# Performance work log

Measured on AMD Instinct MI355X. Metric: run time of the kernel, lower is better.

Reference implementation:

```python
import jax, jax.numpy as jnp
import numpy as np


def _ternarize(p, delta, w):
    # {-w, 0, +w} via threshold mask, matching TrainableTernarize.forward
    return jnp.where(p > delta, w, jnp.where(p < -delta, -w, jnp.zeros_like(p)))


def _ternary_para(p, w):
    # TrainableTernaryPara.forward: delta = 0.05 * max|p|
    delta = 0.05 * jnp.max(jnp.abs(p))
    return _ternarize(p, delta, w)


def _init_scale(p):
    # w init: mean(|p|[|p| > 0.7 * mean|p|])
    a = jnp.abs(p)
    mask = (a > 0.7 * jnp.mean(a)).astype(p.dtype)
    return jnp.sum(a * mask) / jnp.sum(mask)


def setup_inputs() -> dict:
    key = jax.random.key(0)
    k1, k2, k3 = jax.random.split(key, 3)
    B, S, D_IN, D_OUT = 4, 2048, 4096, 4096
    x = jax.random.normal(k1, (B, S, D_IN), dtype=jnp.float32)
    bound = 1.0 / np.sqrt(D_IN)  # nn.Linear default init range
    W = jax.random.uniform(k2, (D_OUT, D_IN), minval=-bound, maxval=bound, dtype=jnp.float32)
    b = jax.random.uniform(k3, (D_OUT,), minval=-bound, maxval=bound, dtype=jnp.float32)
    w_scale = _init_scale(W)
    b_scale = _init_scale(b)
    return {"x": x, "W": W, "w_scale": w_scale, "b": b, "b_scale": b_scale}


def reference(x, W, w_scale, b, b_scale):
    Wt = _ternary_para(W, w_scale)   # [D_OUT, D_IN] in {-w,0,+w}
    bt = _ternary_para(b, b_scale)   # [D_OUT]
    # F.linear(x, Wt, bt) = x @ Wt.T + bt
    return jnp.einsum('bsi,oi->bso', x, Wt) + bt
```

## Files before the change

kernel.cpp:

```cpp
#include <hip/hip_runtime.h>

typedef int v4i __attribute__((ext_vector_type(4)));

#define BM 256
#define BN 256
#define BKB 64
#define NRING 4

#define GLOAD_LDS(gptr, lptr)                                                         \
  __builtin_amdgcn_global_load_lds(                                                   \
      (const __attribute__((address_space(1))) unsigned int*)(gptr),                  \
      (__attribute__((address_space(3))) unsigned int*)(lptr), 16, 0, 0)


__device__ __forceinline__ float max4abs(float4 v) {
  return fmaxf(fmaxf(fabsf(v.x), fabsf(v.y)), fmaxf(fabsf(v.z), fabsf(v.w)));
}

__device__ __forceinline__ int packq4(float4 v, float inv) {
  int b0 = ((int)fminf(127.f, fmaxf(-127.f, rintf(v.x * inv)))) & 255;
  int b1 = ((int)fminf(127.f, fmaxf(-127.f, rintf(v.y * inv)))) & 255;
  int b2 = ((int)fminf(127.f, fmaxf(-127.f, rintf(v.z * inv)))) & 255;
  int b3 = ((int)fminf(127.f, fmaxf(-127.f, rintf(v.w * inv)))) & 255;
  return b0 | (b1 << 8) | (b2 << 16) | (b3 << 24);
}

__global__ void prep1_kernel(const float4* __restrict__ X4,
                             signed char* __restrict__ Q,
                             float* __restrict__ sx, int K, int nrows,
                             const float4* __restrict__ W4, long nW4,
                             const float4* __restrict__ b4, int nb4,
                             unsigned* __restrict__ mx) {
  __shared__ float sm[4];
  const int tid = threadIdx.x;
  const int bid = blockIdx.x;

  if (bid < nrows) {
    const float4* xr = X4 + (size_t)bid * (K / 4);
    float4 v0 = xr[tid], v1 = xr[tid + 256], v2 = xr[tid + 512], v3 = xr[tid + 768];
    float m = fmaxf(fmaxf(max4abs(v0), max4abs(v1)), fmaxf(max4abs(v2), max4abs(v3)));
    for (int off = 32; off > 0; off >>= 1) m = fmaxf(m, __shfl_down(m, off));
    if ((tid & 63) == 0) sm[tid >> 6] = m;
    __syncthreads();
    const float total = fmaxf(fmaxf(sm[0], sm[1]), fmaxf(sm[2], sm[3]));
    const float inv = 127.f / total;
    int* qw = (int*)(Q + (size_t)bid * K);
    qw[tid]       = packq4(v0, inv);
    qw[tid + 256] = packq4(v1, inv);
    qw[tid + 512] = packq4(v2, inv);
    qw[tid + 768] = packq4(v3, inv);
    if (tid == 0) sx[bid] = total * (1.f / 127.f);
    return;
  }

  float m = 0.f;
  const bool isB = (bid == gridDim.x - 1);
  if (!isB) {
    const long wb = bid - nrows;
    const long stride = 1024L * blockDim.x;
    for (long i = wb * blockDim.x + tid; i < nW4; i += stride)
      m = fmaxf(m, max4abs(W4[i]));
  } else {
    for (int i = tid; i < nb4; i += blockDim.x) m = fmaxf(m, max4abs(b4[i]));
  }
  for (int off = 32; off > 0; off >>= 1) m = fmaxf(m, __shfl_down(m, off));
  if ((tid & 63) == 0) sm[tid >> 6] = m;
  __syncthreads();
  if (tid == 0) {
    m = fmaxf(fmaxf(sm[0], sm[1]), fmaxf(sm[2], sm[3]));
    atomicMax(mx + (isB ? 1 : 0), __float_as_uint(m));
  }
}

__global__ void prep_w_kernel(const float4* __restrict__ W4, long nW4,
                              const float4* __restrict__ b4, int nb4,
                              const unsigned* __restrict__ mx,
                              const float* __restrict__ bscale,
                              int* __restrict__ Twi, float4* __restrict__ bt) {
  if (blockIdx.x == gridDim.x - 1) {
    const float delta = 0.05f * __uint_as_float(mx[1]);
    const float s = *bscale;
    for (int i = threadIdx.x; i < nb4; i += blockDim.x) {
      float4 v = b4[i];
      float4 o;
      o.x = v.x > delta ? s : (v.x < -delta ? -s : 0.f);
      o.y = v.y > delta ? s : (v.y < -delta ? -s : 0.f);
      o.z = v.z > delta ? s : (v.z < -delta ? -s : 0.f);
      o.w = v.w > delta ? s : (v.w < -delta ? -s : 0.f);
      bt[i] = o;
    }
    return;
  }
  const float delta = 0.05f * __uint_as_float(mx[0]);
  const long stride = (long)(gridDim.x - 1) * blockDim.x;
  for (long i = blockIdx.x * (long)blockDim.x + threadIdx.x; i < nW4; i += stride) {
    float4 w = W4[i];
    int b0 = w.x > delta ? 1 : (w.x < -delta ? 0xFF : 0);
    int b1 = w.y > delta ? 1 : (w.y < -delta ? 0xFF : 0);
    int b2 = w.z > delta ? 1 : (w.z < -delta ? 0xFF : 0);
    int b3 = w.w > delta ? 1 : (w.w < -delta ? 0xFF : 0);
    Twi[i] = b0 | (b1 << 8) | (b2 << 16) | (b3 << 24);
  }
}

__global__ __launch_bounds__(512, 2) void gemm_tern_i8(
    const signed char* __restrict__ A,
    const signed char* __restrict__ B,
    const float* __restrict__ sx,
    const float* __restrict__ bt,
    const float* __restrict__ wsc,
    float* __restrict__ C,
    int M, int N, int K) {
  __shared__ __align__(16) signed char lds[NRING][2][BM * BKB];

  const int tid = threadIdx.x;
  const int wave = tid >> 6;
  const int lane = tid & 63;
  const int wm = wave >> 2, wn = wave & 3;
  const int quad = lane >> 4;
  const int l16 = lane & 15;

  const unsigned orig = blockIdx.x;
  const unsigned xcd = orig & 7;
  const unsigned r8 = orig >> 3;
  const int by = (int)(xcd * 4 + (r8 & 3));
  const int bx = (int)(r8 >> 2);
  const int bm0 = by * BM;
  const int bn0 = bx * BN;

  const signed char* gA[2];
  const signed char* gB[2];
#pragma unroll
  for (int j = 0; j < 2; ++j) {
    const int idx = j * 512 + tid;
    const int row = idx >> 2;
    const int gch = (idx & 3) ^ ((idx >> 3) & 3);
    gA[j] = A + (size_t)(bm0 + row) * K + gch * 16;
    gB[j] = B + (size_t)(bn0 + row) * K + gch * 16;
  }
  const int ldsbase = wave * 64 * 16;

#define STAGE_A(slot)                                \
  do {                                               \
    signed char* la = &lds[slot][0][ldsbase];        \
    GLOAD_LDS(gA[0], la);                            \
    GLOAD_LDS(gA[1], la + 8192);                     \
    gA[0] += BKB; gA[1] += BKB;                      \
  } while (0)
#define STAGE_B(slot)                                \
  do {                                               \
    signed char* lb = &lds[slot][1][ldsbase];        \
    GLOAD_LDS(gB[0], lb);                            \
    GLOAD_LDS(gB[1], lb + 8192);                     \
    gB[0] += BKB; gB[1] += BKB;                      \
  } while (0)

#define BAR()  do { __builtin_amdgcn_sched_barrier(0); __builtin_amdgcn_s_barrier(); \
                    __builtin_amdgcn_sched_barrier(0); } while (0)
#define WAITLGKM() do { asm volatile("s_waitcnt lgkmcnt(0)" ::: "memory");           \
                        __builtin_amdgcn_sched_barrier(0); } while (0)

  const int kchunk = quad ^ ((l16 >> 1) & 3);
  const int aoff = (wm * 128 + l16) * BKB + kchunk * 16;
  const int boff = (wn * 64 + l16) * BKB + kchunk * 16;

  v4i acc[8][4] = {};

  STAGE_A(0); STAGE_B(0);
  STAGE_A(1); STAGE_B(1);
  STAGE_A(2); STAGE_B(2);
  asm volatile("s_waitcnt vmcnt(8)" ::: "memory");
  BAR();

  const int NT = K / BKB;
  for (int t = 0; t < NT; ++t) {
    const int slot = t & 3;
    const v4i* fA = (const v4i*)&lds[slot][0][aoff];
    const v4i* fB = (const v4i*)&lds[slot][1][boff];
    const bool pf = (t + 3 < NT);
    const int pslot = (t + 3) & 3;
    v4i af[8], bf[4];

    af[0] = fA[0]; af[1] = fA[64]; af[2] = fA[128]; af[3] = fA[192];
    bf[0] = fB[0]; bf[1] = fB[64];
    if (pf) STAGE_A(pslot);
    BAR();
    WAITLGKM();
    __builtin_amdgcn_s_setprio(1);
#pragma unroll
    for (int mt = 0; mt < 4; ++mt)
#pragma unroll
      for (int nt = 0; nt < 2; ++nt)
        acc[mt][nt] = __builtin_amdgcn_mfma_i32_16x16x64_i8(af[mt], bf[nt], acc[mt][nt], 0, 0, 0);
    __builtin_amdgcn_s_setprio(0);
    BAR();

    bf[2] = fB[128]; bf[3] = fB[192];
    if (pf) STAGE_B(pslot);
    BAR();
    WAITLGKM();
    __builtin_amdgcn_s_setprio(1);
#pragma unroll
    for (int mt = 0; mt < 4; ++mt)
#pragma unroll
      for (int nt = 2; nt < 4; ++nt)
        acc[mt][nt] = __builtin_amdgcn_mfma_i32_16x16x64_i8(af[mt], bf[nt], acc[mt][nt], 0, 0, 0);
    __builtin_amdgcn_s_setprio(0);
    BAR();

    af[4] = fA[256]; af[5] = fA[320]; af[6] = fA[384]; af[7] = fA[448];
    BAR();
    WAITLGKM();
    __builtin_amdgcn_s_setprio(1);
#pragma unroll
    for (int mt = 4; mt < 8; ++mt)
#pragma unroll
      for (int nt = 2; nt < 4; ++nt)
        acc[mt][nt] = __builtin_amdgcn_mfma_i32_16x16x64_i8(af[mt], bf[nt], acc[mt][nt], 0, 0, 0);
    __builtin_amdgcn_s_setprio(0);
    BAR();

    asm volatile("s_waitcnt vmcnt(8)" ::: "memory");
    BAR();
    __builtin_amdgcn_s_setprio(1);
#pragma unroll
    for (int mt = 4; mt < 8; ++mt)
#pragma unroll
      for (int nt = 0; nt < 2; ++nt)
        acc[mt][nt] = __builtin_amdgcn_mfma_i32_16x16x64_i8(af[mt], bf[nt], acc[mt][nt], 0, 0, 0);
    __builtin_amdgcn_s_setprio(0);
    BAR();
  }
#undef STAGE_A
#undef STAGE_B
#undef BAR
#undef WAITLGKM

  const float ws = *wsc;
#pragma unroll
  for (int mt = 0; mt < 8; ++mt) {
    const int row = bm0 + wm * 128 + mt * 16 + quad * 4;
    float sc[4];
#pragma unroll
    for (int r = 0; r < 4; ++r) sc[r] = ws * sx[row + r];
#pragma unroll
    for (int nt = 0; nt < 4; ++nt) {
      const int col = bn0 + wn * 64 + nt * 16 + l16;
      const float bias = bt[col];
#pragma unroll
      for (int r = 0; r < 4; ++r)
        C[(size_t)(row + r) * N + col] = sc[r] * (float)acc[mt][nt][r] + bias;
    }
  }
}


extern "C" void kernel_launch(void* const* d_in, const int* in_sizes, int n_in,
                              void* d_out, int out_size, void* d_ws, size_t ws_size,
                              hipStream_t stream) {
  const float* x = (const float*)d_in[0];
  const float* W = (const float*)d_in[1];
  const float* w_scale = (const float*)d_in[2];
  const float* b = (const float*)d_in[3];
  const float* b_scale = (const float*)d_in[4];
  float* out = (float*)d_out;

  const int K = 4096;
  const int N = in_sizes[3];
  const int M = in_sizes[0] / K;

  char* ws = (char*)d_ws;
  signed char* xb = (signed char*)ws;
  signed char* Tw = (signed char*)(ws + (size_t)M * K);
  float* bt = (float*)(ws + (size_t)M * K + (size_t)N * K);
  float* sx = bt + N;
  unsigned* mx = (unsigned*)(sx + M);

  hipMemsetAsync(mx, 0, 8, stream);

  const long nW4 = (long)N * K / 4;
  const int nb4 = N / 4;

  prep1_kernel<<<M + 1024 + 1, 256, 0, stream>>>((const float4*)x, xb, sx, K, M,
                                                 (const float4*)W, nW4,
                                                 (const float4*)b, nb4, mx);

  prep_w_kernel<<<2049, 256, 0, stream>>>((const float4*)W, nW4,
                                          (const float4*)b, nb4, mx, b_scale,
                                          (int*)Tw, (float4*)bt);

  const int nwg = (N / BN) * (M / BM);
  gemm_tern_i8<<<nwg, 512, 0, stream>>>(xb, Tw, sx, bt, w_scale, out, M, N, K);
}
```

Baseline: 406.7 us.

## Switch int8 GEMM to 32x32x32 MFMA with one barrier per K-step

Replaces the 16x16x64 int8 MFMA tiling with 32x32x32 MFMA tiles (4x2 per wave). The old four-phase per-iteration schedule with many barriers becomes a single combined A/B stage, one barrier per K-tile, and double-buffered B fragments loaded one step ahead. The goal is fewer LDS fragment reads per flop and less barrier overhead. The risk is longer MFMA latency chains, higher register pressure from the 16-wide accumulators, and a less coalesced epilogue store pattern.

```diff
diff --git a/kernel.cpp b/kernel.cpp
--- a/kernel.cpp
+++ b/kernel.cpp
@@ -1,6 +1,7 @@
 #include <hip/hip_runtime.h>
 
 typedef int v4i __attribute__((ext_vector_type(4)));
+typedef int v16i __attribute__((ext_vector_type(16)));
 
 #define BM 256
 #define BN 256
@@ -117,8 +118,8 @@
   const int wave = tid >> 6;
   const int lane = tid & 63;
   const int wm = wave >> 2, wn = wave & 3;
-  const int quad = lane >> 4;
-  const int l16 = lane & 15;
+  const int l32 = lane & 31;
+  const int khalf = lane >> 5;
 
   const unsigned orig = blockIdx.x;
   const unsigned xcd = orig & 7;
@@ -140,116 +141,99 @@
   }
   const int ldsbase = wave * 64 * 16;
 
-#define STAGE_A(slot)                                \
+#define STAGE(slot)                                  \
   do {                                               \
     signed char* la = &lds[slot][0][ldsbase];        \
+    signed char* lb = &lds[slot][1][ldsbase];        \
     GLOAD_LDS(gA[0], la);                            \
     GLOAD_LDS(gA[1], la + 8192);                     \
-    gA[0] += BKB; gA[1] += BKB;                      \
-  } while (0)
-#define STAGE_B(slot)                                \
-  do {                                               \
-    signed char* lb = &lds[slot][1][ldsbase];        \
     GLOAD_LDS(gB[0], lb);                            \
     GLOAD_LDS(gB[1], lb + 8192);                     \
+    gA[0] += BKB; gA[1] += BKB;                      \
     gB[0] += BKB; gB[1] += BKB;                      \
   } while (0)
 
-#define BAR()  do { __builtin_amdgcn_sched_barrier(0); __builtin_amdgcn_s_barrier(); \
-                    __builtin_amdgcn_sched_barrier(0); } while (0)
-#define WAITLGKM() do { asm volatile("s_waitcnt lgkmcnt(0)" ::: "memory");           \
-                        __builtin_amdgcn_sched_barrier(0); } while (0)
-
-  const int kchunk = quad ^ ((l16 >> 1) & 3);
-  const int aoff = (wm * 128 + l16) * BKB + kchunk * 16;
-  const int boff = (wn * 64 + l16) * BKB + kchunk * 16;
-
-  v4i acc[8][4] = {};
-
-  STAGE_A(0); STAGE_B(0);
-  STAGE_A(1); STAGE_B(1);
-  STAGE_A(2); STAGE_B(2);
-  asm volatile("s_waitcnt vmcnt(8)" ::: "memory");
-  BAR();
+  const int q = (l32 >> 1) & 3;
+  const int pos0 = (khalf + 0) ^ q;
+  const int pos1 = (khalf + 2) ^ q;
+  const int aoff0 = (wm * 128 + l32) * BKB + pos0 * 16;
+  const int aoff1 = (wm * 128 + l32) * BKB + pos1 * 16;
+  const int boff0 = (wn * 64 + l32) * BKB + pos0 * 16;
+  const int boff1 = (wn * 64 + l32) * BKB + pos1 * 16;
+
+  v16i acc[4][2] = {};
+  v4i bfA[2][2], bfB[2][2];
 
   const int NT = K / BKB;
-  for (int t = 0; t < NT; ++t) {
-    const int slot = t & 3;
-    const v4i* fA = (const v4i*)&lds[slot][0][aoff];
-    const v4i* fB = (const v4i*)&lds[slot][1][boff];
-    const bool pf = (t + 3 < NT);
-    const int pslot = (t + 3) & 3;
-    v4i af[8], bf[4];
-
-    af[0] = fA[0]; af[1] = fA[64]; af[2] = fA[128]; af[3] = fA[192];
-    bf[0] = fB[0]; bf[1] = fB[64];
-    if (pf) STAGE_A(pslot);
-    BAR();
-    WAITLGKM();
-    __builtin_amdgcn_s_setprio(1);
-#pragma unroll
-    for (int mt = 0; mt < 4; ++mt)
-#pragma unroll
-      for (int nt = 0; nt < 2; ++nt)
-        acc[mt][nt] = __builtin_amdgcn_mfma_i32_16x16x64_i8(af[mt], bf[nt], acc[mt][nt], 0, 0, 0);
-    __builtin_amdgcn_s_setprio(0);
-    BAR();
-
-    bf[2] = fB[128]; bf[3] = fB[192];
-    if (pf) STAGE_B(pslot);
-    BAR();
-    WAITLGKM();
-    __builtin_amdgcn_s_setprio(1);
-#pragma unroll
-    for (int mt = 0; mt < 4; ++mt)
-#pragma unroll
-      for (int nt = 2; nt < 4; ++nt)
-        acc[mt][nt] = __builtin_amdgcn_mfma_i32_16x16x64_i8(af[mt], bf[nt], acc[mt][nt], 0, 0, 0);
-    __builtin_amdgcn_s_setprio(0);
-    BAR();
-
-    af[4] = fA[256]; af[5] = fA[320]; af[6] = fA[384]; af[7] = fA[448];
-    BAR();
-    WAITLGKM();
-    __builtin_amdgcn_s_setprio(1);
-#pragma unroll
-    for (int mt = 4; mt < 8; ++mt)
-#pragma unroll
-      for (int nt = 2; nt < 4; ++nt)
-        acc[mt][nt] = __builtin_amdgcn_mfma_i32_16x16x64_i8(af[mt], bf[nt], acc[mt][nt], 0, 0, 0);
-    __builtin_amdgcn_s_setprio(0);
-    BAR();
-
-    asm volatile("s_waitcnt vmcnt(8)" ::: "memory");
-    BAR();
-    __builtin_amdgcn_s_setprio(1);
-#pragma unroll
-    for (int mt = 4; mt < 8; ++mt)
-#pragma unroll
-      for (int nt = 0; nt < 2; ++nt)
-        acc[mt][nt] = __builtin_amdgcn_mfma_i32_16x16x64_i8(af[mt], bf[nt], acc[mt][nt], 0, 0, 0);
-    __builtin_amdgcn_s_setprio(0);
-    BAR();
-  }
-#undef STAGE_A
-#undef STAGE_B
-#undef BAR
-#undef WAITLGKM
+
+  STAGE(0); STAGE(1); STAGE(2);
+  asm volatile("s_waitcnt vmcnt(4)" ::: "memory");
+  asm volatile("s_barrier" ::: "memory");
+
+#pragma unroll
+  for (int nt = 0; nt < 2; ++nt) {
+    bfA[nt][0] = *(const v4i*)(&lds[0][1][0] + boff0 + nt * 2048);
+    bfA[nt][1] = *(const v4i*)(&lds[0][1][0] + boff1 + nt * 2048);
+  }
+
+#define BODY(T, CUR, NXT)                                                              \
+  do {                                                                                 \
+    const int slot_ = (T) & 3;                                                         \
+    if ((T) + 3 < NT) STAGE(((T) + 3) & 3);                                            \
+    const signed char* sa_ = &lds[slot_][0][0];                                        \
+    v4i af_[4][2];                                                                     \
+    _Pragma("unroll")                                                                  \
+    for (int mt = 0; mt < 4; ++mt) {                                                   \
+      af_[mt][0] = *(const v4i*)(sa_ + aoff0 + mt * 2048);                             \
+      af_[mt][1] = *(const v4i*)(sa_ + aoff1 + mt * 2048);                             \
+    }                                                                                  \
+    if ((T) + 1 < NT) {                                                                \
+      const signed char* sbn_ = &lds[((T) + 1) & 3][1][0];                             \
+      _Pragma("unroll")                                                                \
+      for (int nt = 0; nt < 2; ++nt) {                                                 \
+        NXT[nt][0] = *(const v4i*)(sbn_ + boff0 + nt * 2048);                          \
+        NXT[nt][1] = *(const v4i*)(sbn_ + boff1 + nt * 2048);                          \
+      }                                                                                \
+    }                                                                                  \
+    __builtin_amdgcn_s_setprio(1);                                                     \
+    _Pragma("unroll")                                                                  \
+    for (int mt = 0; mt < 4; ++mt)                                                     \
+      _Pragma("unroll")                                                                \
+      for (int nt = 0; nt < 2; ++nt) {                                                 \
+        acc[mt][nt] = __builtin_amdgcn_mfma_i32_32x32x32_i8(af_[mt][0], CUR[nt][0],    \
+                                                            acc[mt][nt], 0, 0, 0);    \
+        acc[mt][nt] = __builtin_amdgcn_mfma_i32_32x32x32_i8(af_[mt][1], CUR[nt][1],    \
+                                                            acc[mt][nt], 0, 0, 0);    \
+      }                                                                                \
+    __builtin_amdgcn_s_setprio(0);                                                     \
+    asm volatile("s_waitcnt vmcnt(4)" ::: "memory");                                   \
+    asm volatile("s_barrier" ::: "memory");                                            \
+  } while (0)
+
+  for (int t = 0; t < NT - 2; t += 2) {
+    BODY(t, bfA, bfB);
+    BODY(t + 1, bfB, bfA);
+  }
+  asm volatile("s_waitcnt vmcnt(0)" ::: "memory");
+  asm volatile("s_barrier" ::: "memory");
+  BODY(NT - 2, bfA, bfB);
+  BODY(NT - 1, bfB, bfA);
+#undef BODY
+#undef STAGE
 
   const float ws = *wsc;
 #pragma unroll
-  for (int mt = 0; mt < 8; ++mt) {
-    const int row = bm0 + wm * 128 + mt * 16 + quad * 4;
-    float sc[4];
-#pragma unroll
-    for (int r = 0; r < 4; ++r) sc[r] = ws * sx[row + r];
-#pragma unroll
-    for (int nt = 0; nt < 4; ++nt) {
-      const int col = bn0 + wn * 64 + nt * 16 + l16;
+  for (int mt = 0; mt < 4; ++mt) {
+    const int rowbase = bm0 + wm * 128 + mt * 32 + 4 * khalf;
+#pragma unroll
+    for (int nt = 0; nt < 2; ++nt) {
+      const int col = bn0 + wn * 64 + nt * 32 + l32;
       const float bias = bt[col];
 #pragma unroll
-      for (int r = 0; r < 4; ++r)
-        C[(size_t)(row + r) * N + col] = sc[r] * (float)acc[mt][nt][r] + bias;
+      for (int r = 0; r < 16; ++r) {
+        const int row = rowbase + (r & 3) + 8 * (r >> 2);
+        C[(size_t)row * N + col] = ws * sx[row] * (float)acc[mt][nt][r] + bias;
+      }
     }
   }
 }
```

New measurement: 413.1 us. About the same (+1.6%).

## Restructure int8 GEMM main loop into double-buffered register pipeline with pinned scheduling

Applied to the files above, without the earlier changes.

Replaces the four-phase barrier-heavy main loop with a software-pipelined loop unrolled by two. A and B register fragments are double-buffered (afA/afB, bfP/bfQ), so LDS reads for the next tile overlap MFMAs on the current one. sched_group_barrier pins the interleaving of global loads, LDS reads and MFMAs, and there is now a single barrier per k-step instead of several. The loop count is hardcoded to K=4096 (64 tiles), so the kernel only works for that K and raises register pressure from the extra fragment buffers.

```diff
diff --git a/kernel.cpp b/kernel.cpp
--- a/kernel.cpp
+++ b/kernel.cpp
@@ -128,113 +128,141 @@
   const int bm0 = by * BM;
   const int bn0 = bx * BN;
 
-  const signed char* gA[2];
-  const signed char* gB[2];
-#pragma unroll
-  for (int j = 0; j < 2; ++j) {
-    const int idx = j * 512 + tid;
-    const int row = idx >> 2;
-    const int gch = (idx & 3) ^ ((idx >> 3) & 3);
-    gA[j] = A + (size_t)(bm0 + row) * K + gch * 16;
-    gB[j] = B + (size_t)(bn0 + row) * K + gch * 16;
+  const signed char *gA0, *gA1, *gB0, *gB1;
+  {
+    const int i0 = tid, i1 = 512 + tid;
+    const int r0 = i0 >> 2, r1 = i1 >> 2;
+    const int c0 = (i0 & 3) ^ ((i0 >> 3) & 3);
+    const int c1 = (i1 & 3) ^ ((i1 >> 3) & 3);
+    gA0 = A + (size_t)(bm0 + r0) * K + c0 * 16;
+    gA1 = A + (size_t)(bm0 + r1) * K + c1 * 16;
+    gB0 = B + (size_t)(bn0 + r0) * K + c0 * 16;
+    gB1 = B + (size_t)(bn0 + r1) * K + c1 * 16;
   }
   const int ldsbase = wave * 64 * 16;
 
-#define STAGE_A(slot)                                \
+#define STAGE(slot)                                  \
   do {                                               \
     signed char* la = &lds[slot][0][ldsbase];        \
-    GLOAD_LDS(gA[0], la);                            \
-    GLOAD_LDS(gA[1], la + 8192);                     \
-    gA[0] += BKB; gA[1] += BKB;                      \
-  } while (0)
-#define STAGE_B(slot)                                \
-  do {                                               \
     signed char* lb = &lds[slot][1][ldsbase];        \
-    GLOAD_LDS(gB[0], lb);                            \
-    GLOAD_LDS(gB[1], lb + 8192);                     \
-    gB[0] += BKB; gB[1] += BKB;                      \
-  } while (0)
-
-#define BAR()  do { __builtin_amdgcn_sched_barrier(0); __builtin_amdgcn_s_barrier(); \
-                    __builtin_amdgcn_sched_barrier(0); } while (0)
-#define WAITLGKM() do { asm volatile("s_waitcnt lgkmcnt(0)" ::: "memory");           \
-                        __builtin_amdgcn_sched_barrier(0); } while (0)
+    GLOAD_LDS(gA0, la);                              \
+    GLOAD_LDS(gA1, la + 8192);                       \
+    GLOAD_LDS(gB0, lb);                              \
+    GLOAD_LDS(gB1, lb + 8192);                       \
+    gA0 += BKB; gA1 += BKB; gB0 += BKB; gB1 += BKB;  \
+  } while (0)
 
   const int kchunk = quad ^ ((l16 >> 1) & 3);
   const int aoff = (wm * 128 + l16) * BKB + kchunk * 16;
   const int boff = (wn * 64 + l16) * BKB + kchunk * 16;
 
+  v4i afA[4], afB[4], bfP[4], bfQ[4];
   v4i acc[8][4] = {};
 
-  STAGE_A(0); STAGE_B(0);
-  STAGE_A(1); STAGE_B(1);
-  STAGE_A(2); STAGE_B(2);
-  asm volatile("s_waitcnt vmcnt(8)" ::: "memory");
-  BAR();
-
-  const int NT = K / BKB;
-  for (int t = 0; t < NT; ++t) {
-    const int slot = t & 3;
-    const v4i* fA = (const v4i*)&lds[slot][0][aoff];
-    const v4i* fB = (const v4i*)&lds[slot][1][boff];
-    const bool pf = (t + 3 < NT);
-    const int pslot = (t + 3) & 3;
-    v4i af[8], bf[4];
-
-    af[0] = fA[0]; af[1] = fA[64]; af[2] = fA[128]; af[3] = fA[192];
-    bf[0] = fB[0]; bf[1] = fB[64];
-    if (pf) STAGE_A(pslot);
-    BAR();
-    WAITLGKM();
-    __builtin_amdgcn_s_setprio(1);
-#pragma unroll
-    for (int mt = 0; mt < 4; ++mt)
-#pragma unroll
-      for (int nt = 0; nt < 2; ++nt)
-        acc[mt][nt] = __builtin_amdgcn_mfma_i32_16x16x64_i8(af[mt], bf[nt], acc[mt][nt], 0, 0, 0);
-    __builtin_amdgcn_s_setprio(0);
-    BAR();
-
-    bf[2] = fB[128]; bf[3] = fB[192];
-    if (pf) STAGE_B(pslot);
-    BAR();
-    WAITLGKM();
-    __builtin_amdgcn_s_setprio(1);
-#pragma unroll
-    for (int mt = 0; mt < 4; ++mt)
-#pragma unroll
-      for (int nt = 2; nt < 4; ++nt)
-        acc[mt][nt] = __builtin_amdgcn_mfma_i32_16x16x64_i8(af[mt], bf[nt], acc[mt][nt], 0, 0, 0);
-    __builtin_amdgcn_s_setprio(0);
-    BAR();
-
-    af[4] = fA[256]; af[5] = fA[320]; af[6] = fA[384]; af[7] = fA[448];
-    BAR();
-    WAITLGKM();
-    __builtin_amdgcn_s_setprio(1);
-#pragma unroll
-    for (int mt = 4; mt < 8; ++mt)
-#pragma unroll
-      for (int nt = 2; nt < 4; ++nt)
-        acc[mt][nt] = __builtin_amdgcn_mfma_i32_16x16x64_i8(af[mt], bf[nt], acc[mt][nt], 0, 0, 0);
-    __builtin_amdgcn_s_setprio(0);
-    BAR();
-
-    asm volatile("s_waitcnt vmcnt(8)" ::: "memory");
-    BAR();
-    __builtin_amdgcn_s_setprio(1);
-#pragma unroll
-    for (int mt = 4; mt < 8; ++mt)
-#pragma unroll
-      for (int nt = 0; nt < 2; ++nt)
-        acc[mt][nt] = __builtin_amdgcn_mfma_i32_16x16x64_i8(af[mt], bf[nt], acc[mt][nt], 0, 0, 0);
-    __builtin_amdgcn_s_setprio(0);
-    BAR();
-  }
-#undef STAGE_A
-#undef STAGE_B
-#undef BAR
-#undef WAITLGKM
+#define RD_AFA(T)                                         \
+  do {                                                    \
+    const signed char* s_ = &lds[(T) & 3][0][0];          \
+    afA[0] = *(const v4i*)(s_ + aoff);                    \
+    afA[1] = *(const v4i*)(s_ + aoff + 1024);             \
+    afA[2] = *(const v4i*)(s_ + aoff + 2048);             \
+    afA[3] = *(const v4i*)(s_ + aoff + 3072);             \
+  } while (0)
+#define RD_AFB(T)                                         \
+  do {                                                    \
+    const signed char* s_ = &lds[(T) & 3][0][0];          \
+    afB[0] = *(const v4i*)(s_ + aoff + 4096);             \
+    afB[1] = *(const v4i*)(s_ + aoff + 5120);             \
+    afB[2] = *(const v4i*)(s_ + aoff + 6144);             \
+    afB[3] = *(const v4i*)(s_ + aoff + 7168);             \
+  } while (0)
+#define RD_BF(DST, T)                                     \
+  do {                                                    \
+    const signed char* s_ = &lds[(T) & 3][1][0];          \
+    DST[0] = *(const v4i*)(s_ + boff);                    \
+    DST[1] = *(const v4i*)(s_ + boff + 1024);             \
+    DST[2] = *(const v4i*)(s_ + boff + 2048);             \
+    DST[3] = *(const v4i*)(s_ + boff + 3072);             \
+  } while (0)
+
+#define MM(AF, BF, MB)                                                        \
+  do {                                                                        \
+    __builtin_amdgcn_s_setprio(1);                                            \
+    _Pragma("unroll")                                                         \
+    for (int mt = 0; mt < 4; ++mt)                                            \
+      _Pragma("unroll")                                                       \
+      for (int nt = 0; nt < 4; ++nt)                                          \
+        acc[(MB) + mt][nt] = __builtin_amdgcn_mfma_i32_16x16x64_i8(           \
+            AF[mt], BF[nt], acc[(MB) + mt][nt], 0, 0, 0);                     \
+    __builtin_amdgcn_s_setprio(0);                                            \
+  } while (0)
+
+#define SGB(m, n) __builtin_amdgcn_sched_group_barrier((m), (n), 0)
+#define PIN_FULL() do { SGB(0x20,4); SGB(0x100,4); SGB(0x8,16); SGB(0x100,8); SGB(0x8,16); } while (0)
+#define PIN_NOST() do { SGB(0x100,4); SGB(0x8,16); SGB(0x100,8); SGB(0x8,16); } while (0)
+
+#define VMB(n)                                            \
+  do {                                                    \
+    asm volatile("s_waitcnt vmcnt(" #n ")" ::: "memory"); \
+    asm volatile("s_barrier" ::: "memory");               \
+  } while (0)
+
+  STAGE(0); STAGE(1); STAGE(2);
+  asm volatile("s_waitcnt vmcnt(4)" ::: "memory");
+  asm volatile("s_barrier" ::: "memory");
+  RD_AFA(0);
+  RD_BF(bfP, 0);
+
+  for (int t = 0; t < 60; t += 2) {
+    STAGE((t + 3) & 3);
+    RD_AFB(t);
+    MM(afA, bfP, 0);
+    RD_AFA(t + 1);
+    RD_BF(bfQ, t + 1);
+    MM(afB, bfP, 4);
+    PIN_FULL();
+    VMB(4);
+    STAGE((t + 4) & 3);
+    RD_AFB(t + 1);
+    MM(afA, bfQ, 0);
+    RD_AFA(t + 2);
+    RD_BF(bfP, t + 2);
+    MM(afB, bfQ, 4);
+    PIN_FULL();
+    VMB(4);
+  }
+  STAGE(3);
+  RD_AFB(60);
+  MM(afA, bfP, 0);
+  RD_AFA(61);
+  RD_BF(bfQ, 61);
+  MM(afB, bfP, 4);
+  PIN_FULL();
+  VMB(4);
+  RD_AFB(61);
+  MM(afA, bfQ, 0);
+  RD_AFA(62);
+  RD_BF(bfP, 62);
+  MM(afB, bfQ, 4);
+  PIN_NOST();
+  VMB(0);
+  RD_AFB(62);
+  MM(afA, bfP, 0);
+  RD_AFA(63);
+  RD_BF(bfQ, 63);
+  MM(afB, bfP, 4);
+  RD_AFB(63);
+  MM(afA, bfQ, 0);
+  MM(afB, bfQ, 4);
+
+#undef STAGE
+#undef RD_AFA
+#undef RD_AFB
+#undef RD_BF
+#undef MM
+#undef SGB
+#undef PIN_FULL
+#undef PIN_NOST
+#undef VMB
 
   const float ws = *wsc;
 #pragma unroll
```

New measurement: 398.6 us. 1.02x faster.

## Replace LDS-staged int8 GEMM pipeline with direct global-to-register double buffering

Applied to the files above, without the earlier changes.

Removes the shared-memory ring buffer and its global_load_lds staging. Each wave now loads its A and B MFMA fragments straight from global memory into registers, double-buffered across two k-steps, with sched_group_barrier interleaving the loads and MFMAs. The goal is to cut LDS traffic and the many block barriers. In exchange, operands shared between waves are no longer reused through LDS, so redundant global/L2 traffic rises and register pressure grows. The loop count is hardcoded to 62+2 iterations, which assumes K=4096.

```diff
diff --git a/kernel.cpp b/kernel.cpp
--- a/kernel.cpp
+++ b/kernel.cpp
@@ -5,12 +5,6 @@
 #define BM 256
 #define BN 256
 #define BKB 64
-#define NRING 4
-
-#define GLOAD_LDS(gptr, lptr)                                                         \
-  __builtin_amdgcn_global_load_lds(                                                   \
-      (const __attribute__((address_space(1))) unsigned int*)(gptr),                  \
-      (__attribute__((address_space(3))) unsigned int*)(lptr), 16, 0, 0)
 
 
 __device__ __forceinline__ float max4abs(float4 v) {
@@ -111,8 +105,6 @@
     const float* __restrict__ wsc,
     float* __restrict__ C,
     int M, int N, int K) {
-  __shared__ __align__(16) signed char lds[NRING][2][BM * BKB];
-
   const int tid = threadIdx.x;
   const int wave = tid >> 6;
   const int lane = tid & 63;
@@ -128,113 +120,61 @@
   const int bm0 = by * BM;
   const int bn0 = bx * BN;
 
-  const signed char* gA[2];
-  const signed char* gB[2];
-#pragma unroll
-  for (int j = 0; j < 2; ++j) {
-    const int idx = j * 512 + tid;
-    const int row = idx >> 2;
-    const int gch = (idx & 3) ^ ((idx >> 3) & 3);
-    gA[j] = A + (size_t)(bm0 + row) * K + gch * 16;
-    gB[j] = B + (size_t)(bn0 + row) * K + gch * 16;
-  }
-  const int ldsbase = wave * 64 * 16;
-
-#define STAGE_A(slot)                                \
-  do {                                               \
-    signed char* la = &lds[slot][0][ldsbase];        \
-    GLOAD_LDS(gA[0], la);                            \
-    GLOAD_LDS(gA[1], la + 8192);                     \
-    gA[0] += BKB; gA[1] += BKB;                      \
+  const unsigned aoff0 = (unsigned)((bm0 + wm * 128 + l16) * K + quad * 16);
+  const unsigned boff0 = (unsigned)((bn0 + wn * 64 + l16) * K + quad * 16);
+
+  const signed char* Ak = A;
+  const signed char* Bk = B;
+
+  v4i afP[8], bfP[4], afQ[8], bfQ[4];
+  v4i acc[8][4] = {};
+
+#define LDF(AF, BF)                                                   \
+  do {                                                                \
+    _Pragma("unroll")                                                 \
+    for (int mt = 0; mt < 8; ++mt)                                    \
+      AF[mt] = *(const v4i*)(Ak + ((unsigned)(mt * 16) * K + aoff0)); \
+    _Pragma("unroll")                                                 \
+    for (int nt = 0; nt < 4; ++nt)                                    \
+      BF[nt] = *(const v4i*)(Bk + ((unsigned)(nt * 16) * K + boff0)); \
+    Ak += BKB;                                                        \
+    Bk += BKB;                                                        \
   } while (0)
-#define STAGE_B(slot)                                \
-  do {                                               \
-    signed char* lb = &lds[slot][1][ldsbase];        \
-    GLOAD_LDS(gB[0], lb);                            \
-    GLOAD_LDS(gB[1], lb + 8192);                     \
-    gB[0] += BKB; gB[1] += BKB;                      \
+
+#define MM(AF, BF)                                                            \
+  do {                                                                        \
+    __builtin_amdgcn_s_setprio(1);                                            \
+    _Pragma("unroll")                                                         \
+    for (int mt = 0; mt < 8; ++mt)                                            \
+      _Pragma("unroll")                                                       \
+      for (int nt = 0; nt < 4; ++nt)                                          \
+        acc[mt][nt] = __builtin_amdgcn_mfma_i32_16x16x64_i8(                  \
+            AF[mt], BF[nt], acc[mt][nt], 0, 0, 0);                            \
+    __builtin_amdgcn_s_setprio(0);                                            \
   } while (0)
 
-#define BAR()  do { __builtin_amdgcn_sched_barrier(0); __builtin_amdgcn_s_barrier(); \
-                    __builtin_amdgcn_sched_barrier(0); } while (0)
-#define WAITLGKM() do { asm volatile("s_waitcnt lgkmcnt(0)" ::: "memory");           \
-                        __builtin_amdgcn_sched_barrier(0); } while (0)
-
-  const int kchunk = quad ^ ((l16 >> 1) & 3);
-  const int aoff = (wm * 128 + l16) * BKB + kchunk * 16;
-  const int boff = (wn * 64 + l16) * BKB + kchunk * 16;
-
-  v4i acc[8][4] = {};
-
-  STAGE_A(0); STAGE_B(0);
-  STAGE_A(1); STAGE_B(1);
-  STAGE_A(2); STAGE_B(2);
-  asm volatile("s_waitcnt vmcnt(8)" ::: "memory");
-  BAR();
-
-  const int NT = K / BKB;
-  for (int t = 0; t < NT; ++t) {
-    const int slot = t & 3;
-    const v4i* fA = (const v4i*)&lds[slot][0][aoff];
-    const v4i* fB = (const v4i*)&lds[slot][1][boff];
-    const bool pf = (t + 3 < NT);
-    const int pslot = (t + 3) & 3;
-    v4i af[8], bf[4];
-
-    af[0] = fA[0]; af[1] = fA[64]; af[2] = fA[128]; af[3] = fA[192];
-    bf[0] = fB[0]; bf[1] = fB[64];
-    if (pf) STAGE_A(pslot);
-    BAR();
-    WAITLGKM();
-    __builtin_amdgcn_s_setprio(1);
-#pragma unroll
-    for (int mt = 0; mt < 4; ++mt)
-#pragma unroll
-      for (int nt = 0; nt < 2; ++nt)
-        acc[mt][nt] = __builtin_amdgcn_mfma_i32_16x16x64_i8(af[mt], bf[nt], acc[mt][nt], 0, 0, 0);
-    __builtin_amdgcn_s_setprio(0);
-    BAR();
-
-    bf[2] = fB[128]; bf[3] = fB[192];
-    if (pf) STAGE_B(pslot);
-    BAR();
-    WAITLGKM();
-    __builtin_amdgcn_s_setprio(1);
-#pragma unroll
-    for (int mt = 0; mt < 4; ++mt)
-#pragma unroll
-      for (int nt = 2; nt < 4; ++nt)
-        acc[mt][nt] = __builtin_amdgcn_mfma_i32_16x16x64_i8(af[mt], bf[nt], acc[mt][nt], 0, 0, 0);
-    __builtin_amdgcn_s_setprio(0);
-    BAR();
-
-    af[4] = fA[256]; af[5] = fA[320]; af[6] = fA[384]; af[7] = fA[448];
-    BAR();
-    WAITLGKM();
-    __builtin_amdgcn_s_setprio(1);
-#pragma unroll
-    for (int mt = 4; mt < 8; ++mt)
-#pragma unroll
-      for (int nt = 2; nt < 4; ++nt)
-        acc[mt][nt] = __builtin_amdgcn_mfma_i32_16x16x64_i8(af[mt], bf[nt], acc[mt][nt], 0, 0, 0);
-    __builtin_amdgcn_s_setprio(0);
-    BAR();
-
-    asm volatile("s_waitcnt vmcnt(8)" ::: "memory");
-    BAR();
-    __builtin_amdgcn_s_setprio(1);
-#pragma unroll
-    for (int mt = 4; mt < 8; ++mt)
-#pragma unroll
-      for (int nt = 0; nt < 2; ++nt)
-        acc[mt][nt] = __builtin_amdgcn_mfma_i32_16x16x64_i8(af[mt], bf[nt], acc[mt][nt], 0, 0, 0);
-    __builtin_amdgcn_s_setprio(0);
-    BAR();
-  }
-#undef STAGE_A
-#undef STAGE_B
-#undef BAR
-#undef WAITLGKM
+#define SGB(m, n) __builtin_amdgcn_sched_group_barrier((m), (n), 0)
+#define PIN() do { SGB(0x20, 12); SGB(0x8, 32); } while (0)
+
+  LDF(afP, bfP);
+  for (int t = 0; t < 62; t += 2) {
+    LDF(afQ, bfQ);
+    MM(afP, bfP);
+    PIN();
+    LDF(afP, bfP);
+    MM(afQ, bfQ);
+    PIN();
+    if ((t & 7) == 6) __builtin_amdgcn_s_barrier();
+  }
+  LDF(afQ, bfQ);
+  MM(afP, bfP);
+  PIN();
+  MM(afQ, bfQ);
+
+#undef LDF
+#undef MM
+#undef SGB
+#undef PIN
 
   const float ws = *wsc;
 #pragma unroll
```

After: 688.5 us. +69.3%, slower.
